# Performance work log

Hardware: AMD Instinct MI355X
Metric: run time of the kernel (lower is better)

Reference implementation:

```python
import jax, jax.numpy as jnp
import numpy as np

B, S, EMB, HEAD = 8, 2048, 2048, 128
ROPE_BASE = 10000.0


def _rope(x):
    # x: [B, S, D]; standard rotate-half rotary position embedding
    d = x.shape[-1]
    half = d // 2
    inv_freq = 1.0 / (ROPE_BASE ** (jnp.arange(half, dtype=jnp.float32) / half))  # [half]
    ang = jnp.arange(x.shape[-2], dtype=jnp.float32)[:, None] * inv_freq           # [S, half]
    cos, sin = jnp.cos(ang), jnp.sin(ang)
    x1, x2 = x[..., :half], x[..., half:]
    return jnp.concatenate([x1 * cos - x2 * sin, x1 * sin + x2 * cos], axis=-1)


def setup_inputs() -> dict:
    key = jax.random.key(0)
    ks = jax.random.split(key, 7)
    sc = 1.0 / np.sqrt(EMB)
    return {
        "x": jax.random.normal(ks[0], (B, S, EMB), dtype=jnp.float32),
        "Wq": jax.random.normal(ks[1], (EMB, HEAD), dtype=jnp.float32) * sc,
        "bq": jax.random.normal(ks[2], (HEAD,), dtype=jnp.float32) * 0.02,
        "Wk": jax.random.normal(ks[3], (EMB, HEAD), dtype=jnp.float32) * sc,
        "bk": jax.random.normal(ks[4], (HEAD,), dtype=jnp.float32) * 0.02,
        "Wv": jax.random.normal(ks[5], (EMB, HEAD), dtype=jnp.float32) * sc,
        "bv": jax.random.normal(ks[6], (HEAD,), dtype=jnp.float32) * 0.02,
    }


def reference(x, Wq, bq, Wk, bk, Wv, bv):
    # single-head causal self-attention with RoPE (cache=None path)
    q = _rope(x @ Wq + bq)            # [B, S, HEAD]
    k = _rope(x @ Wk + bk)            # [B, S, HEAD]
    v = x @ Wv + bv                   # [B, S, HEAD]
    scale = 1.0 / jnp.sqrt(jnp.float32(HEAD))
    scores = jnp.einsum('bqd,bkd->bqk', q, k) * scale   # [B, S, S]
    causal = jnp.tril(jnp.ones((S, S), dtype=bool))
    scores = jnp.where(causal, scores, -jnp.inf)
    weights = jax.nn.softmax(scores, axis=-1)
    return jnp.einsum('bqk,bkd->bqd', weights, v)       # [B, S, HEAD]
```

## Files before the change

kernel.cpp:

```cpp
#include <hip/hip_runtime.h>

typedef __bf16 bf16;
typedef __bf16 bf16x8 __attribute__((ext_vector_type(8)));
typedef float f32x4 __attribute__((ext_vector_type(4)));

#define S_LEN 2048
#define EMBD 2048
#define HD 128

__device__ inline void gload16(const void* g, void* l) {
  __builtin_amdgcn_global_load_lds(
      (const __attribute__((address_space(1))) unsigned int*)g,
      (__attribute__((address_space(3))) unsigned int*)l, 16, 0, 0);
}

__global__ __launch_bounds__(256) void k_prep(const float* __restrict__ Wq,
                                              const float* __restrict__ Wk,
                                              const float* __restrict__ Wv,
                                              bf16* __restrict__ wt) {
  __shared__ bf16 wls[64 * 72];

  const int t = threadIdx.x;
  const int bid = blockIdx.x;
  const int mat = bid >> 6;
  const int nt = bid & 1;
  const int kt = (bid & 63) >> 1;
  const int k0 = kt * 64, n0 = nt * 64;
  const float* W = (mat == 0) ? Wq : ((mat == 1) ? Wk : Wv);

#pragma unroll
  for (int i = 0; i < 4; ++i) {
    int e = i * 256 + t;
    int r = e >> 4, c4 = e & 15;
    float4 v = *(const float4*)(W + (size_t)(k0 + r) * HD + n0 + c4 * 4);
    union { bf16 h[4]; uint2 u; } p;
    p.h[0] = (bf16)v.x; p.h[1] = (bf16)v.y;
    p.h[2] = (bf16)v.z; p.h[3] = (bf16)v.w;
    *(uint2*)&wls[r * 72 + c4 * 4] = p.u;
  }
  __syncthreads();
#pragma unroll
  for (int i = 0; i < 2; ++i) {
    int slot = i * 256 + t;
    int n_loc = slot >> 3, kq = slot & 7;
    int n = n0 + n_loc;
    int kbase = (kq * 8) ^ ((n & 7) << 3);
    union { bf16 h[8]; uint4 u; } p;
#pragma unroll
    for (int j = 0; j < 8; ++j) p.h[j] = wls[(kbase + j) * 72 + n_loc];
    *(uint4*)&wt[(size_t)(mat * HD + n) * EMBD + k0 + kq * 8] = p.u;
  }
}

__global__ __launch_bounds__(256, 3) void k_qkv(
    const float* __restrict__ x, const bf16* __restrict__ wt,
    const float* __restrict__ bq, const float* __restrict__ bk,
    const float* __restrict__ bv, bf16* __restrict__ Qw, bf16* __restrict__ Kw,
    bf16* __restrict__ Vtw) {
  __shared__ __align__(16) bf16 xs[2][64 * 72];
  __shared__ __align__(16) bf16 wts[2][128 * 64];

  const int tid = threadIdx.x;
  const int lane = tid & 63;
  const int wave = tid >> 6;
  const int wm = wave >> 1;
  const int wn = wave & 1;
  const int l15 = lane & 15;
  const int lh = lane >> 4;

  const int bid = blockIdx.x;
  const int g = bid >> 3;
  const int by = g % 3;
  const int mt = (bid & 7) + 8 * (g / 3);
  const int row0 = mt * 64;

  f32x4 acc[2][4];
#pragma unroll
  for (int mf = 0; mf < 2; ++mf)
#pragma unroll
    for (int f = 0; f < 4; ++f) acc[mf][f] = {};

  int xr_[4], xk_[4];
  const float* xp_[4];
#pragma unroll
  for (int i = 0; i < 4; ++i) {
    int e = (i * 256 + tid) * 4;
    xr_[i] = e >> 6;
    xk_[i] = e & 63;
    xp_[i] = x + (size_t)(row0 + xr_[i]) * EMBD + xk_[i];
  }
  const bf16* wp_[4];
  int we_[4];
#pragma unroll
  for (int i = 0; i < 4; ++i) {
    int e = (i * 256 + tid) * 8;
    int np = e >> 6, k = e & 63;
    wp_[i] = wt + (size_t)(by * 128 + np) * EMBD + k;
    we_[i] = e;
  }

  auto stage_issue = [&](int ks, int buf, float4* xr) {
#pragma unroll
    for (int i = 0; i < 4; ++i) xr[i] = *(const float4*)(xp_[i] + ks * 64);
#pragma unroll
    for (int i = 0; i < 4; ++i) gload16(wp_[i] + ks * 64, &wts[buf][we_[i]]);
  };
  auto xwrite = [&](int buf, const float4* xr) {
#pragma unroll
    for (int i = 0; i < 4; ++i) {
      union { bf16 h[4]; uint2 u; } p;
      p.h[0] = (bf16)xr[i].x; p.h[1] = (bf16)xr[i].y;
      p.h[2] = (bf16)xr[i].z; p.h[3] = (bf16)xr[i].w;
      *(uint2*)&xs[buf][xr_[i] * 72 + xk_[i]] = p.u;
    }
  };

  {
    float4 xr[4];
    stage_issue(0, 0, xr);
    xwrite(0, xr);
  }
  __syncthreads();

  for (int ks = 0; ks < EMBD / 64; ++ks) {
    const int c = ks & 1, pbuf = c ^ 1;
    float4 xr[4];
    if (ks < EMBD / 64 - 1) stage_issue(ks + 1, pbuf, xr);

#pragma unroll
    for (int kk = 0; kk < 2; ++kk) {
      bf16x8 a[2];
#pragma unroll
      for (int mf = 0; mf < 2; ++mf)
        a[mf] = *(const bf16x8*)&xs[c][(wm * 32 + mf * 16 + l15) * 72 + kk * 32 + lh * 8];
#pragma unroll
      for (int f = 0; f < 4; ++f) {
        int col = (f & 1) * 16 + (f >> 1) * 64 + wn * 32 + l15;
        int klin = (kk * 32 + lh * 8) ^ ((col & 7) << 3);
        bf16x8 b = *(const bf16x8*)&wts[c][col * 64 + klin];
#pragma unroll
        for (int mf = 0; mf < 2; ++mf)
          acc[mf][f] =
              __builtin_amdgcn_mfma_f32_16x16x32_bf16(a[mf], b, acc[mf][f], 0, 0, 0);
      }
    }

    if (ks < EMBD / 64 - 1) xwrite(pbuf, xr);
    __syncthreads();
  }

  const int bb = row0 >> 11;
  const int s0 = row0 & (S_LEN - 1);

  if (by < 2) {
    const float* bias = (by == 0) ? bq : bk;
#pragma unroll
    for (int fp = 0; fp < 2; ++fp) {
      const int colA = wn * 32 + fp * 16 + l15;
      const int colB = colA + 64;
      float biasA = bias[colA], biasB = bias[colB];
      float invf = exp2f((float)colA * -0.20762050593046014f);
#pragma unroll
      for (int mf = 0; mf < 2; ++mf) {
#pragma unroll
        for (int r = 0; r < 4; ++r) {
          int s = s0 + wm * 32 + mf * 16 + lh * 4 + r;
          float xa = acc[mf][fp][r] + biasA;
          float xb = acc[mf][fp + 2][r] + biasB;
          float sn, cs;
          sincosf((float)s * invf, &sn, &cs);
          float oa = xa * cs - xb * sn;
          float ob = xa * sn + xb * cs;
          if (by == 0) {
            Qw[(size_t)(bb * S_LEN + s) * HD + colA] = (bf16)oa;
            Qw[(size_t)(bb * S_LEN + s) * HD + colB] = (bf16)ob;
          } else {
            int sw = (s & 7) << 3;
            Kw[(size_t)(bb * S_LEN + s) * HD + (colA ^ sw)] = (bf16)oa;
            Kw[(size_t)(bb * S_LEN + s) * HD + (colB ^ sw)] = (bf16)ob;
          }
        }
      }
    }
  } else {
    __syncthreads();
    bf16* vstage = &xs[0][0];
#pragma unroll
    for (int f = 0; f < 4; ++f) {
      int dv = (f & 1) * 16 + (f >> 1) * 64 + wn * 32 + l15;
      float biasV = bv[dv];
#pragma unroll
      for (int mf = 0; mf < 2; ++mf)
#pragma unroll
        for (int r = 0; r < 4; ++r) {
          int mrow = wm * 32 + mf * 16 + lh * 4 + r;
          vstage[dv * 72 + mrow] = (bf16)(acc[mf][f][r] + biasV);
        }
    }
    __syncthreads();
#pragma unroll
    for (int i = 0; i < 4; ++i) {
      int c = i * 256 + tid;
      int dv = c >> 3, kq = c & 7;
      uint4 v = *(const uint4*)&vstage[dv * 72 + kq * 8];
      int slot = (kq * 8) ^ ((dv & 7) << 3);
      *(uint4*)&Vtw[((size_t)(bb * HD + dv) << 11) + s0 + slot] = v;
    }
  }
}

__global__ __launch_bounds__(512) void k_attn(
    const bf16* __restrict__ Qw, const bf16* __restrict__ Kw,
    const bf16* __restrict__ Vtw, float* __restrict__ out) {
  __shared__ __align__(16) char arena[131072];
  __shared__ __align__(16) bf16 pld[8 * 16 * 72];
  __shared__ float mls[64], lls[64];

  bf16(*kls)[64 * 128] = (bf16(*)[64 * 128])arena;
  bf16(*vls)[128 * 64] = (bf16(*)[128 * 64])(arena + 65536);
  float* oml = (float*)arena;

  const int tid = threadIdx.x;
  const int lane = tid & 63;
  const int wave = tid >> 6;
  const int grp = wave >> 2;
  const int w4 = wave & 3;
  const int l15 = lane & 15;
  const int lh = lane >> 4;
  const int t256 = tid & 255;

  const int bid = blockIdx.x;
  const int batch = bid & 7;
  const int qt = 31 - (bid >> 3);
  const int qbase = qt * 64;
  const int nt = qt + 1;
  const int mysteps = (nt - grp + 1) >> 1;
  const int maxst = (nt + 1) >> 1;

  const bf16* kbat = Kw + (size_t)(batch * S_LEN) * HD;
  const bf16* vbat = Vtw + ((size_t)(batch * HD) << 11);

  auto stage = [&](int t, int buf) {
    bf16* kdst = kls[grp * 2 + buf];
    bf16* vdst = vls[grp * 2 + buf];
    const bf16* kbase = kbat + (size_t)(t * 64) * HD;
#pragma unroll
    for (int i = 0; i < 4; ++i) {
      int c = i * 256 + t256;
      gload16(kbase + c * 8, kdst + c * 8);
    }
    const bf16* vbase = vbat + t * 64;
#pragma unroll
    for (int i = 0; i < 4; ++i) {
      int c = i * 256 + t256;
      int dv = c >> 3, kq = (c & 7) * 8;
      gload16(vbase + ((size_t)dv << 11) + kq, vdst + c * 8);
    }
  };

  bf16x8 qa[4];
  {
    const bf16* qptr = Qw + (size_t)(batch * S_LEN + qbase + w4 * 16 + l15) * HD;
#pragma unroll
    for (int kk = 0; kk < 4; ++kk) qa[kk] = *(const bf16x8*)(qptr + kk * 32 + lh * 8);
  }

  f32x4 o[8];
#pragma unroll
  for (int i = 0; i < 8; ++i) o[i] = {};
  float m[4], lsum[4];
#pragma unroll
  for (int r = 0; r < 4; ++r) { m[r] = -__builtin_inff(); lsum[r] = 0.f; }

  const float scale = 0.08838834764831845f;

  if (mysteps > 0) stage(grp, 0);
  __syncthreads();

  for (int i = 0; i < maxst; ++i) {
    if (i + 1 < mysteps) stage(2 * (i + 1) + grp, (i + 1) & 1);
    if (i < mysteps) {
      const int t = 2 * i + grp;
      const int buf = grp * 2 + (i & 1);
      const int kv0 = t * 64;

      f32x4 sc[4];
#pragma unroll
      for (int nf = 0; nf < 4; ++nf) sc[nf] = {};
      __builtin_amdgcn_s_setprio(1);
#pragma unroll
      for (int kk = 0; kk < 4; ++kk) {
#pragma unroll
        for (int nf = 0; nf < 4; ++nf) {
          int row = nf * 16 + l15;
          int dlin = (kk * 32 + lh * 8) ^ ((row & 7) << 3);
          bf16x8 kb = *(const bf16x8*)&kls[buf][row * 128 + dlin];
          sc[nf] = __builtin_amdgcn_mfma_f32_16x16x32_bf16(qa[kk], kb, sc[nf], 0, 0, 0);
        }
      }
      __builtin_amdgcn_s_setprio(0);

      const bool diag = (t == qt);
      const int qg0 = qbase + w4 * 16 + lh * 4;
#pragma unroll
      for (int nf = 0; nf < 4; ++nf) {
        int kvg = kv0 + nf * 16 + l15;
#pragma unroll
        for (int r = 0; r < 4; ++r) {
          float v = sc[nf][r] * scale;
          if (diag && kvg > qg0 + r) v = -__builtin_inff();
          sc[nf][r] = v;
        }
      }

      float mnew[4], alpha[4], rs[4];
#pragma unroll
      for (int r = 0; r < 4; ++r) {
        float v = fmaxf(fmaxf(sc[0][r], sc[1][r]), fmaxf(sc[2][r], sc[3][r]));
#pragma unroll
        for (int sh = 1; sh < 16; sh <<= 1) v = fmaxf(v, __shfl_xor(v, sh));
        mnew[r] = fmaxf(m[r], v);
        alpha[r] = __expf(m[r] - mnew[r]);
        m[r] = mnew[r];
        rs[r] = 0.f;
      }

      bf16* pw = &pld[wave * 16 * 72];
#pragma unroll
      for (int nf = 0; nf < 4; ++nf)
#pragma unroll
        for (int r = 0; r < 4; ++r) {
          float p = __expf(sc[nf][r] - mnew[r]);
          bf16 pb = (bf16)p;
          pw[(lh * 4 + r) * 72 + nf * 16 + l15] = pb;
          rs[r] += (float)pb;
        }
#pragma unroll
      for (int r = 0; r < 4; ++r) {
        float v = rs[r];
#pragma unroll
        for (int sh = 1; sh < 16; sh <<= 1) v += __shfl_xor(v, sh);
        lsum[r] = lsum[r] * alpha[r] + v;
      }
#pragma unroll
      for (int i2 = 0; i2 < 8; ++i2)
#pragma unroll
        for (int r = 0; r < 4; ++r) o[i2][r] *= alpha[r];

      __builtin_amdgcn_s_setprio(1);
#pragma unroll
      for (int kkv = 0; kkv < 2; ++kkv) {
        bf16x8 pa = *(const bf16x8*)&pw[l15 * 72 + kkv * 32 + lh * 8];
#pragma unroll
        for (int df = 0; df < 8; ++df) {
          int dv = df * 16 + l15;
          int klin = (kkv * 32 + lh * 8) ^ ((dv & 7) << 3);
          bf16x8 vb = *(const bf16x8*)&vls[buf][dv * 64 + klin];
          o[df] = __builtin_amdgcn_mfma_f32_16x16x32_bf16(pa, vb, o[df], 0, 0, 0);
        }
      }
      __builtin_amdgcn_s_setprio(0);
    }
    __syncthreads();
  }

  if (grp == 1) {
#pragma unroll
    for (int df = 0; df < 8; ++df)
#pragma unroll
      for (int r = 0; r < 4; ++r)
        oml[(w4 * 16 + lh * 4 + r) * 128 + df * 16 + l15] = o[df][r];
    if (l15 == 0) {
#pragma unroll
      for (int r = 0; r < 4; ++r) {
        mls[w4 * 16 + lh * 4 + r] = m[r];
        lls[w4 * 16 + lh * 4 + r] = lsum[r];
      }
    }
  }
  __syncthreads();
  if (grp == 0) {
#pragma unroll
    for (int r = 0; r < 4; ++r) {
      int row = w4 * 16 + lh * 4 + r;
      float m1 = mls[row], l1 = lls[row];
      float mm = fmaxf(m[r], m1);
      float s0 = __expf(m[r] - mm);
      float s1 = __expf(m1 - mm);
      float inv = 1.0f / (lsum[r] * s0 + l1 * s1);
      float* op = out + (size_t)(batch * S_LEN + qbase + row) * HD;
#pragma unroll
      for (int df = 0; df < 8; ++df)
        op[df * 16 + l15] =
            (o[df][r] * s0 + oml[row * 128 + df * 16 + l15] * s1) * inv;
    }
  }
}

extern "C" void kernel_launch(void* const* d_in, const int* in_sizes, int n_in,
                              void* d_out, int out_size, void* d_ws, size_t ws_size,
                              hipStream_t stream) {
  const float* x = (const float*)d_in[0];
  const float* Wq = (const float*)d_in[1];
  const float* bq = (const float*)d_in[2];
  const float* Wk = (const float*)d_in[3];
  const float* bk = (const float*)d_in[4];
  const float* Wv = (const float*)d_in[5];
  const float* bv = (const float*)d_in[6];
  float* out = (float*)d_out;

  char* ws = (char*)d_ws;
  bf16* wt  = (bf16*)(ws);
  bf16* Qw  = (bf16*)(ws + (size_t)(2u << 20));
  bf16* Kw  = (bf16*)(ws + (size_t)(6u << 20));
  bf16* Vtw = (bf16*)(ws + (size_t)(10u << 20));

  hipLaunchKernelGGL(k_prep, dim3(192), dim3(256), 0, stream, Wq, Wk, Wv, wt);
  hipLaunchKernelGGL(k_qkv, dim3(768), dim3(256), 0, stream, x, wt, bq, bk, bv,
                     Qw, Kw, Vtw);
  hipLaunchKernelGGL(k_attn, dim3(256), dim3(512), 0, stream, Qw, Kw, Vtw, out);
}
```

Measured before the change: 102.6 us.

## Load x fragments directly from global into registers, bypassing LDS staging

The QKV projection kernel now has each lane read its MFMA A-operand fragments of x straight from global memory into registers. It converts them to bf16 in-register and prefetches the next k-step's fragments, instead of staging x through a double-buffered LDS tile. This removes the LDS writes and reads for x and frees that shared memory, which may help occupancy. In exchange, the two waves sharing the same rows (wn=0/1) now both load them from global, and the per-lane strided float4 reads are less coalesced than the old staging pattern. The V epilogue reuses the weight LDS buffer and drops a barrier; this relies on the final loop barrier to make that reuse safe.

```diff
diff --git a/kernel.cpp b/kernel.cpp
--- a/kernel.cpp
+++ b/kernel.cpp
@@ -57,7 +57,6 @@
     const float* __restrict__ bq, const float* __restrict__ bk,
     const float* __restrict__ bv, bf16* __restrict__ Qw, bf16* __restrict__ Kw,
     bf16* __restrict__ Vtw) {
-  __shared__ __align__(16) bf16 xs[2][64 * 72];
   __shared__ __align__(16) bf16 wts[2][128 * 64];
 
   const int tid = threadIdx.x;
@@ -80,15 +79,8 @@
 #pragma unroll
     for (int f = 0; f < 4; ++f) acc[mf][f] = {};
 
-  int xr_[4], xk_[4];
-  const float* xp_[4];
-#pragma unroll
-  for (int i = 0; i < 4; ++i) {
-    int e = (i * 256 + tid) * 4;
-    xr_[i] = e >> 6;
-    xk_[i] = e & 63;
-    xp_[i] = x + (size_t)(row0 + xr_[i]) * EMBD + xk_[i];
-  }
+  const float* xa = x + (size_t)(row0 + wm * 32 + l15) * EMBD + lh * 8;
+
   const bf16* wp_[4];
   int we_[4];
 #pragma unroll
@@ -99,53 +91,63 @@
     we_[i] = e;
   }
 
-  auto stage_issue = [&](int ks, int buf, float4* xr) {
-#pragma unroll
-    for (int i = 0; i < 4; ++i) xr[i] = *(const float4*)(xp_[i] + ks * 64);
-#pragma unroll
-    for (int i = 0; i < 4; ++i) gload16(wp_[i] + ks * 64, &wts[buf][we_[i]]);
-  };
-  auto xwrite = [&](int buf, const float4* xr) {
-#pragma unroll
-    for (int i = 0; i < 4; ++i) {
-      union { bf16 h[4]; uint2 u; } p;
-      p.h[0] = (bf16)xr[i].x; p.h[1] = (bf16)xr[i].y;
-      p.h[2] = (bf16)xr[i].z; p.h[3] = (bf16)xr[i].w;
-      *(uint2*)&xs[buf][xr_[i] * 72 + xk_[i]] = p.u;
-    }
-  };
-
-  {
-    float4 xr[4];
-    stage_issue(0, 0, xr);
-    xwrite(0, xr);
-  }
+  float4 an[4][2];
+#pragma unroll
+  for (int mf = 0; mf < 2; ++mf)
+#pragma unroll
+    for (int kk = 0; kk < 2; ++kk) {
+      const float* p = xa + (size_t)(mf * 16) * EMBD + kk * 32;
+      an[mf * 2 + kk][0] = *(const float4*)(p);
+      an[mf * 2 + kk][1] = *(const float4*)(p + 4);
+    }
+#pragma unroll
+  for (int i = 0; i < 4; ++i) gload16(wp_[i], &wts[0][we_[i]]);
   __syncthreads();
 
   for (int ks = 0; ks < EMBD / 64; ++ks) {
-    const int c = ks & 1, pbuf = c ^ 1;
-    float4 xr[4];
-    if (ks < EMBD / 64 - 1) stage_issue(ks + 1, pbuf, xr);
+    const int cur = ks & 1;
+    if (ks + 1 < EMBD / 64) {
+#pragma unroll
+      for (int i = 0; i < 4; ++i)
+        gload16(wp_[i] + (ks + 1) * 64, &wts[cur ^ 1][we_[i]]);
+    }
+
+    bf16x8 ab[2][2];
+#pragma unroll
+    for (int mf = 0; mf < 2; ++mf)
+#pragma unroll
+      for (int kk = 0; kk < 2; ++kk) {
+        bf16x8 v;
+        const float4 a0 = an[mf * 2 + kk][0];
+        const float4 a1 = an[mf * 2 + kk][1];
+        v[0] = (bf16)a0.x; v[1] = (bf16)a0.y; v[2] = (bf16)a0.z; v[3] = (bf16)a0.w;
+        v[4] = (bf16)a1.x; v[5] = (bf16)a1.y; v[6] = (bf16)a1.z; v[7] = (bf16)a1.w;
+        ab[mf][kk] = v;
+      }
+    if (ks + 1 < EMBD / 64) {
+#pragma unroll
+      for (int mf = 0; mf < 2; ++mf)
+#pragma unroll
+        for (int kk = 0; kk < 2; ++kk) {
+          const float* p = xa + (size_t)(mf * 16) * EMBD + (ks + 1) * 64 + kk * 32;
+          an[mf * 2 + kk][0] = *(const float4*)(p);
+          an[mf * 2 + kk][1] = *(const float4*)(p + 4);
+        }
+    }
 
 #pragma unroll
     for (int kk = 0; kk < 2; ++kk) {
-      bf16x8 a[2];
-#pragma unroll
-      for (int mf = 0; mf < 2; ++mf)
-        a[mf] = *(const bf16x8*)&xs[c][(wm * 32 + mf * 16 + l15) * 72 + kk * 32 + lh * 8];
 #pragma unroll
       for (int f = 0; f < 4; ++f) {
         int col = (f & 1) * 16 + (f >> 1) * 64 + wn * 32 + l15;
         int klin = (kk * 32 + lh * 8) ^ ((col & 7) << 3);
-        bf16x8 b = *(const bf16x8*)&wts[c][col * 64 + klin];
+        bf16x8 b = *(const bf16x8*)&wts[cur][col * 64 + klin];
 #pragma unroll
         for (int mf = 0; mf < 2; ++mf)
           acc[mf][f] =
-              __builtin_amdgcn_mfma_f32_16x16x32_bf16(a[mf], b, acc[mf][f], 0, 0, 0);
-      }
-    }
-
-    if (ks < EMBD / 64 - 1) xwrite(pbuf, xr);
+              __builtin_amdgcn_mfma_f32_16x16x32_bf16(ab[mf][kk], b, acc[mf][f], 0, 0, 0);
+      }
+    }
     __syncthreads();
   }
 
@@ -165,12 +167,12 @@
 #pragma unroll
         for (int r = 0; r < 4; ++r) {
           int s = s0 + wm * 32 + mf * 16 + lh * 4 + r;
-          float xa = acc[mf][fp][r] + biasA;
-          float xb = acc[mf][fp + 2][r] + biasB;
+          float xa_ = acc[mf][fp][r] + biasA;
+          float xb_ = acc[mf][fp + 2][r] + biasB;
           float sn, cs;
           sincosf((float)s * invf, &sn, &cs);
-          float oa = xa * cs - xb * sn;
-          float ob = xa * sn + xb * cs;
+          float oa = xa_ * cs - xb_ * sn;
+          float ob = xa_ * sn + xb_ * cs;
           if (by == 0) {
             Qw[(size_t)(bb * S_LEN + s) * HD + colA] = (bf16)oa;
             Qw[(size_t)(bb * S_LEN + s) * HD + colB] = (bf16)ob;
@@ -183,8 +185,7 @@
       }
     }
   } else {
-    __syncthreads();
-    bf16* vstage = &xs[0][0];
+    bf16* vstage = &wts[0][0];
 #pragma unroll
     for (int f = 0; f < 4; ++f) {
       int dv = (f & 1) * 16 + (f >> 1) * 64 + wn * 32 + l15;
```

Result: slower. 160.0 us (+55.9%).

## Split QKV projection tile across eight waves and remap blocks per XCD

Applied to the files above, without the earlier changes.

The QKV GEMM kernel goes from 256 to 512 threads per block. Each of the eight waves now computes a 32x32 output sub-tile instead of 32x64, which halves per-thread accumulators and per-thread load counts. Block indices are remapped so each XCD handles a contiguous range of row tiles, with all three Q/K/V column groups for those rows kept together, which should improve L2 reuse of x. The V transpose staging now reuses the weight LDS buffer, dropping one barrier. The costs are more LDS fragment reads per MFMA and heavier barrier traffic with eight waves per block.

```diff
diff --git a/kernel.cpp b/kernel.cpp
--- a/kernel.cpp
+++ b/kernel.cpp
@@ -52,7 +52,7 @@
   }
 }
 
-__global__ __launch_bounds__(256, 3) void k_qkv(
+__global__ __launch_bounds__(512, 6) void k_qkv(
     const float* __restrict__ x, const bf16* __restrict__ wt,
     const float* __restrict__ bq, const float* __restrict__ bk,
     const float* __restrict__ bv, bf16* __restrict__ Qw, bf16* __restrict__ Kw,
@@ -63,37 +63,38 @@
   const int tid = threadIdx.x;
   const int lane = tid & 63;
   const int wave = tid >> 6;
-  const int wm = wave >> 1;
-  const int wn = wave & 1;
+  const int wm = wave >> 2;
+  const int wn = wave & 3;
   const int l15 = lane & 15;
   const int lh = lane >> 4;
 
   const int bid = blockIdx.x;
-  const int g = bid >> 3;
-  const int by = g % 3;
-  const int mt = (bid & 7) + 8 * (g / 3);
+  const int xcd = bid & 7;
+  const int idx = bid >> 3;
+  const int by = idx % 3;
+  const int mt = xcd * 32 + idx / 3;
   const int row0 = mt * 64;
 
-  f32x4 acc[2][4];
+  f32x4 acc[2][2];
 #pragma unroll
   for (int mf = 0; mf < 2; ++mf)
 #pragma unroll
-    for (int f = 0; f < 4; ++f) acc[mf][f] = {};
-
-  int xr_[4], xk_[4];
-  const float* xp_[4];
-#pragma unroll
-  for (int i = 0; i < 4; ++i) {
-    int e = (i * 256 + tid) * 4;
+    for (int f = 0; f < 2; ++f) acc[mf][f] = {};
+
+  int xr_[2], xk_[2];
+  const float* xp_[2];
+#pragma unroll
+  for (int i = 0; i < 2; ++i) {
+    int e = (i * 512 + tid) * 4;
     xr_[i] = e >> 6;
     xk_[i] = e & 63;
     xp_[i] = x + (size_t)(row0 + xr_[i]) * EMBD + xk_[i];
   }
-  const bf16* wp_[4];
-  int we_[4];
-#pragma unroll
-  for (int i = 0; i < 4; ++i) {
-    int e = (i * 256 + tid) * 8;
+  const bf16* wp_[2];
+  int we_[2];
+#pragma unroll
+  for (int i = 0; i < 2; ++i) {
+    int e = (i * 512 + tid) * 8;
     int np = e >> 6, k = e & 63;
     wp_[i] = wt + (size_t)(by * 128 + np) * EMBD + k;
     we_[i] = e;
@@ -101,13 +102,13 @@
 
   auto stage_issue = [&](int ks, int buf, float4* xr) {
 #pragma unroll
-    for (int i = 0; i < 4; ++i) xr[i] = *(const float4*)(xp_[i] + ks * 64);
-#pragma unroll
-    for (int i = 0; i < 4; ++i) gload16(wp_[i] + ks * 64, &wts[buf][we_[i]]);
+    for (int i = 0; i < 2; ++i) xr[i] = *(const float4*)(xp_[i] + ks * 64);
+#pragma unroll
+    for (int i = 0; i < 2; ++i) gload16(wp_[i] + ks * 64, &wts[buf][we_[i]]);
   };
   auto xwrite = [&](int buf, const float4* xr) {
 #pragma unroll
-    for (int i = 0; i < 4; ++i) {
+    for (int i = 0; i < 2; ++i) {
       union { bf16 h[4]; uint2 u; } p;
       p.h[0] = (bf16)xr[i].x; p.h[1] = (bf16)xr[i].y;
       p.h[2] = (bf16)xr[i].z; p.h[3] = (bf16)xr[i].w;
@@ -116,28 +117,28 @@
   };
 
   {
-    float4 xr[4];
+    float4 xr[2];
     stage_issue(0, 0, xr);
     xwrite(0, xr);
   }
   __syncthreads();
 
   for (int ks = 0; ks < EMBD / 64; ++ks) {
-    const int c = ks & 1, pbuf = c ^ 1;
-    float4 xr[4];
-    if (ks < EMBD / 64 - 1) stage_issue(ks + 1, pbuf, xr);
+    const int cur = ks & 1;
+    float4 xr[2];
+    if (ks + 1 < EMBD / 64) stage_issue(ks + 1, cur ^ 1, xr);
 
 #pragma unroll
     for (int kk = 0; kk < 2; ++kk) {
       bf16x8 a[2];
 #pragma unroll
       for (int mf = 0; mf < 2; ++mf)
-        a[mf] = *(const bf16x8*)&xs[c][(wm * 32 + mf * 16 + l15) * 72 + kk * 32 + lh * 8];
-#pragma unroll
-      for (int f = 0; f < 4; ++f) {
-        int col = (f & 1) * 16 + (f >> 1) * 64 + wn * 32 + l15;
-        int klin = (kk * 32 + lh * 8) ^ ((col & 7) << 3);
-        bf16x8 b = *(const bf16x8*)&wts[c][col * 64 + klin];
+        a[mf] = *(const bf16x8*)&xs[cur][(wm * 32 + mf * 16 + l15) * 72 + kk * 32 + lh * 8];
+      const int klin = (kk * 32 + lh * 8) ^ ((l15 & 7) << 3);
+#pragma unroll
+      for (int f = 0; f < 2; ++f) {
+        int col = f * 64 + wn * 16 + l15;
+        bf16x8 b = *(const bf16x8*)&wts[cur][col * 64 + klin];
 #pragma unroll
         for (int mf = 0; mf < 2; ++mf)
           acc[mf][f] =
@@ -145,7 +146,7 @@
       }
     }
 
-    if (ks < EMBD / 64 - 1) xwrite(pbuf, xr);
+    if (ks + 1 < EMBD / 64) xwrite(cur ^ 1, xr);
     __syncthreads();
   }
 
@@ -154,40 +155,36 @@
 
   if (by < 2) {
     const float* bias = (by == 0) ? bq : bk;
-#pragma unroll
-    for (int fp = 0; fp < 2; ++fp) {
-      const int colA = wn * 32 + fp * 16 + l15;
-      const int colB = colA + 64;
-      float biasA = bias[colA], biasB = bias[colB];
-      float invf = exp2f((float)colA * -0.20762050593046014f);
-#pragma unroll
-      for (int mf = 0; mf < 2; ++mf) {
-#pragma unroll
-        for (int r = 0; r < 4; ++r) {
-          int s = s0 + wm * 32 + mf * 16 + lh * 4 + r;
-          float xa = acc[mf][fp][r] + biasA;
-          float xb = acc[mf][fp + 2][r] + biasB;
-          float sn, cs;
-          sincosf((float)s * invf, &sn, &cs);
-          float oa = xa * cs - xb * sn;
-          float ob = xa * sn + xb * cs;
-          if (by == 0) {
-            Qw[(size_t)(bb * S_LEN + s) * HD + colA] = (bf16)oa;
-            Qw[(size_t)(bb * S_LEN + s) * HD + colB] = (bf16)ob;
-          } else {
-            int sw = (s & 7) << 3;
-            Kw[(size_t)(bb * S_LEN + s) * HD + (colA ^ sw)] = (bf16)oa;
-            Kw[(size_t)(bb * S_LEN + s) * HD + (colB ^ sw)] = (bf16)ob;
-          }
+    const int colA = wn * 16 + l15;
+    const int colB = colA + 64;
+    float biasA = bias[colA], biasB = bias[colB];
+    float invf = exp2f((float)colA * -0.20762050593046014f);
+#pragma unroll
+    for (int mf = 0; mf < 2; ++mf) {
+#pragma unroll
+      for (int r = 0; r < 4; ++r) {
+        int s = s0 + wm * 32 + mf * 16 + lh * 4 + r;
+        float xa_ = acc[mf][0][r] + biasA;
+        float xb_ = acc[mf][1][r] + biasB;
+        float sn, cs;
+        sincosf((float)s * invf, &sn, &cs);
+        float oa = xa_ * cs - xb_ * sn;
+        float ob = xa_ * sn + xb_ * cs;
+        if (by == 0) {
+          Qw[(size_t)(bb * S_LEN + s) * HD + colA] = (bf16)oa;
+          Qw[(size_t)(bb * S_LEN + s) * HD + colB] = (bf16)ob;
+        } else {
+          int sw = (s & 7) << 3;
+          Kw[(size_t)(bb * S_LEN + s) * HD + (colA ^ sw)] = (bf16)oa;
+          Kw[(size_t)(bb * S_LEN + s) * HD + (colB ^ sw)] = (bf16)ob;
         }
       }
     }
   } else {
-    __syncthreads();
-    bf16* vstage = &xs[0][0];
-#pragma unroll
-    for (int f = 0; f < 4; ++f) {
-      int dv = (f & 1) * 16 + (f >> 1) * 64 + wn * 32 + l15;
+    bf16* vstage = &wts[0][0];
+#pragma unroll
+    for (int f = 0; f < 2; ++f) {
+      int dv = f * 64 + wn * 16 + l15;
       float biasV = bv[dv];
 #pragma unroll
       for (int mf = 0; mf < 2; ++mf)
@@ -199,8 +196,8 @@
     }
     __syncthreads();
 #pragma unroll
-    for (int i = 0; i < 4; ++i) {
-      int c = i * 256 + tid;
+    for (int i = 0; i < 2; ++i) {
+      int c = i * 512 + tid;
       int dv = c >> 3, kq = c & 7;
       uint4 v = *(const uint4*)&vstage[dv * 72 + kq * 8];
       int slot = (kq * 8) ^ ((dv & 7) << 3);
@@ -416,7 +413,7 @@
   bf16* Vtw = (bf16*)(ws + (size_t)(10u << 20));
 
   hipLaunchKernelGGL(k_prep, dim3(192), dim3(256), 0, stream, Wq, Wk, Wv, wt);
-  hipLaunchKernelGGL(k_qkv, dim3(768), dim3(256), 0, stream, x, wt, bq, bk, bv,
+  hipLaunchKernelGGL(k_qkv, dim3(768), dim3(512), 0, stream, x, wt, bq, bk, bv,
                      Qw, Kw, Vtw);
   hipLaunchKernelGGL(k_attn, dim3(256), dim3(512), 0, stream, Qw, Kw, Vtw, out);
 }
```

Result: no change. 100.9 us (-1.7%).

## Restructure QKV projection with 128-wide K tiles, single LDS buffer and XCD-aware mapping

Applied to the files above, without the earlier changes.

The QKV projection main loop now works on 128-wide K tiles with a single LDS buffer instead of double-buffered 64-wide tiles. The next x tile is prefetched into registers during compute, while the weight tile's global-to-LDS load is issued only after a barrier. Blocks are remapped so that each XCD handles a contiguous range of row tiles, MFMA sections are wrapped in s_setprio, and the occupancy hint is dropped from launch_bounds. This halves the number of loop iterations and barriers and aims for better L2 locality per XCD. The cost is that the weight-load latency is no longer overlapped with compute, and the loop adds an extra barrier per iteration.

```diff
diff --git a/kernel.cpp b/kernel.cpp
--- a/kernel.cpp
+++ b/kernel.cpp
@@ -52,13 +52,13 @@
   }
 }
 
-__global__ __launch_bounds__(256, 3) void k_qkv(
+__global__ __launch_bounds__(256) void k_qkv(
     const float* __restrict__ x, const bf16* __restrict__ wt,
     const float* __restrict__ bq, const float* __restrict__ bk,
     const float* __restrict__ bv, bf16* __restrict__ Qw, bf16* __restrict__ Kw,
     bf16* __restrict__ Vtw) {
-  __shared__ __align__(16) bf16 xs[2][64 * 72];
-  __shared__ __align__(16) bf16 wts[2][128 * 64];
+  __shared__ __align__(16) bf16 xs[64 * 136];
+  __shared__ __align__(16) bf16 wts[128 * 128];
 
   const int tid = threadIdx.x;
   const int lane = tid & 63;
@@ -69,9 +69,10 @@
   const int lh = lane >> 4;
 
   const int bid = blockIdx.x;
-  const int g = bid >> 3;
-  const int by = g % 3;
-  const int mt = (bid & 7) + 8 * (g / 3);
+  const int xcd = bid & 7;
+  const int idx = bid >> 3;
+  const int by = idx % 3;
+  const int mt = xcd * 32 + idx / 3;
   const int row0 = mt * 64;
 
   f32x4 acc[2][4];
@@ -80,73 +81,81 @@
 #pragma unroll
     for (int f = 0; f < 4; ++f) acc[mf][f] = {};
 
-  int xr_[4], xk_[4];
-  const float* xp_[4];
-#pragma unroll
-  for (int i = 0; i < 4; ++i) {
+  int xr_[8], xk_[8];
+  const float* xp_[8];
+#pragma unroll
+  for (int i = 0; i < 8; ++i) {
     int e = (i * 256 + tid) * 4;
-    xr_[i] = e >> 6;
-    xk_[i] = e & 63;
+    xr_[i] = e >> 7;
+    xk_[i] = e & 127;
     xp_[i] = x + (size_t)(row0 + xr_[i]) * EMBD + xk_[i];
   }
-  const bf16* wp_[4];
-  int we_[4];
-#pragma unroll
-  for (int i = 0; i < 4; ++i) {
+  const bf16* wp_[8];
+  int we_[8];
+#pragma unroll
+  for (int i = 0; i < 8; ++i) {
     int e = (i * 256 + tid) * 8;
-    int np = e >> 6, k = e & 63;
+    int np = e >> 7, k = e & 127;
     wp_[i] = wt + (size_t)(by * 128 + np) * EMBD + k;
     we_[i] = e;
   }
 
-  auto stage_issue = [&](int ks, int buf, float4* xr) {
-#pragma unroll
-    for (int i = 0; i < 4; ++i) xr[i] = *(const float4*)(xp_[i] + ks * 64);
-#pragma unroll
-    for (int i = 0; i < 4; ++i) gload16(wp_[i] + ks * 64, &wts[buf][we_[i]]);
+  auto xload = [&](int ks, float4* xr) {
+#pragma unroll
+    for (int i = 0; i < 8; ++i) xr[i] = *(const float4*)(xp_[i] + ks * 128);
   };
-  auto xwrite = [&](int buf, const float4* xr) {
-#pragma unroll
-    for (int i = 0; i < 4; ++i) {
+  auto xwrite = [&](const float4* xr) {
+#pragma unroll
+    for (int i = 0; i < 8; ++i) {
       union { bf16 h[4]; uint2 u; } p;
       p.h[0] = (bf16)xr[i].x; p.h[1] = (bf16)xr[i].y;
       p.h[2] = (bf16)xr[i].z; p.h[3] = (bf16)xr[i].w;
-      *(uint2*)&xs[buf][xr_[i] * 72 + xk_[i]] = p.u;
+      *(uint2*)&xs[xr_[i] * 136 + xk_[i]] = p.u;
     }
   };
+  auto wstage = [&](int ks) {
+#pragma unroll
+    for (int i = 0; i < 8; ++i) gload16(wp_[i] + ks * 128, &wts[we_[i]]);
+  };
 
   {
-    float4 xr[4];
-    stage_issue(0, 0, xr);
-    xwrite(0, xr);
+    float4 xr[8];
+    xload(0, xr);
+    wstage(0);
+    xwrite(xr);
   }
   __syncthreads();
 
-  for (int ks = 0; ks < EMBD / 64; ++ks) {
-    const int c = ks & 1, pbuf = c ^ 1;
-    float4 xr[4];
-    if (ks < EMBD / 64 - 1) stage_issue(ks + 1, pbuf, xr);
-
-#pragma unroll
-    for (int kk = 0; kk < 2; ++kk) {
+  float4 xnext[8];
+  for (int ks = 0; ks < 16; ++ks) {
+    if (ks + 1 < 16) xload(ks + 1, xnext);
+
+    __builtin_amdgcn_s_setprio(1);
+#pragma unroll
+    for (int kk = 0; kk < 4; ++kk) {
       bf16x8 a[2];
 #pragma unroll
       for (int mf = 0; mf < 2; ++mf)
-        a[mf] = *(const bf16x8*)&xs[c][(wm * 32 + mf * 16 + l15) * 72 + kk * 32 + lh * 8];
+        a[mf] = *(const bf16x8*)&xs[(wm * 32 + mf * 16 + l15) * 136 + kk * 32 + lh * 8];
 #pragma unroll
       for (int f = 0; f < 4; ++f) {
         int col = (f & 1) * 16 + (f >> 1) * 64 + wn * 32 + l15;
         int klin = (kk * 32 + lh * 8) ^ ((col & 7) << 3);
-        bf16x8 b = *(const bf16x8*)&wts[c][col * 64 + klin];
+        bf16x8 b = *(const bf16x8*)&wts[col * 128 + klin];
 #pragma unroll
         for (int mf = 0; mf < 2; ++mf)
           acc[mf][f] =
               __builtin_amdgcn_mfma_f32_16x16x32_bf16(a[mf], b, acc[mf][f], 0, 0, 0);
       }
     }
-
-    if (ks < EMBD / 64 - 1) xwrite(pbuf, xr);
+    __builtin_amdgcn_s_setprio(0);
+
     __syncthreads();
+    if (ks + 1 < 16) {
+      wstage(ks + 1);
+      xwrite(xnext);
+      __syncthreads();
+    }
   }
 
   const int bb = row0 >> 11;
@@ -165,12 +174,12 @@
 #pragma unroll
         for (int r = 0; r < 4; ++r) {
           int s = s0 + wm * 32 + mf * 16 + lh * 4 + r;
-          float xa = acc[mf][fp][r] + biasA;
-          float xb = acc[mf][fp + 2][r] + biasB;
+          float xa_ = acc[mf][fp][r] + biasA;
+          float xb_ = acc[mf][fp + 2][r] + biasB;
           float sn, cs;
           sincosf((float)s * invf, &sn, &cs);
-          float oa = xa * cs - xb * sn;
-          float ob = xa * sn + xb * cs;
+          float oa = xa_ * cs - xb_ * sn;
+          float ob = xa_ * sn + xb_ * cs;
           if (by == 0) {
             Qw[(size_t)(bb * S_LEN + s) * HD + colA] = (bf16)oa;
             Qw[(size_t)(bb * S_LEN + s) * HD + colB] = (bf16)ob;
@@ -184,7 +193,7 @@
     }
   } else {
     __syncthreads();
-    bf16* vstage = &xs[0][0];
+    bf16* vstage = &wts[0];
 #pragma unroll
     for (int f = 0; f < 4; ++f) {
       int dv = (f & 1) * 16 + (f >> 1) * 64 + wn * 32 + l15;
```

Result: slower. 115.5 us (+12.5%).
